# Kernel tuning notes

Measured on AMD Instinct MI355X. Metric: run time of the kernel, lower is better.

## Reference

```python
import jax, jax.numpy as jnp
import numpy as np

EMB = 1024
HEADS = 16
HEAD_DIM = EMB // HEADS
EPS = 1e-5


def gelu_tanh(x):
    c = jnp.sqrt(jnp.asarray(2.0 / jnp.pi, x.dtype))
    return 0.5 * x * (1.0 + jnp.tanh(c * (x + 0.044715 * x ** 3)))


def layernorm(x, scale, shift):
    mean = jnp.mean(x, axis=-1, keepdims=True)
    var = jnp.mean((x - mean) ** 2, axis=-1, keepdims=True)  # unbiased=False
    return scale * (x - mean) / jnp.sqrt(var + EPS) + shift


def setup_inputs() -> dict:
    key = jax.random.key(0)
    ks = jax.random.split(key, 12)
    d, dff = EMB, 4 * EMB
    sd = 1.0 / np.sqrt(d)
    inp = {
        "x": jax.random.normal(ks[0], (2, 2048, d), jnp.float32),
        "Wq": jax.random.normal(ks[1], (d, d), jnp.float32) * sd,
        "Wk": jax.random.normal(ks[2], (d, d), jnp.float32) * sd,
        "Wv": jax.random.normal(ks[3], (d, d), jnp.float32) * sd,
        "Wo": jax.random.normal(ks[4], (d, d), jnp.float32) * sd,
        "bo": jnp.zeros((d,), jnp.float32),
        "W1": jax.random.normal(ks[5], (d, dff), jnp.float32) * sd,
        "b1": jnp.zeros((dff,), jnp.float32),
        "W2": jax.random.normal(ks[6], (dff, d), jnp.float32) * (1.0 / np.sqrt(dff)),
        "b2": jnp.zeros((d,), jnp.float32),
        "g1": jnp.ones((d,), jnp.float32),
        "s1": jnp.zeros((d,), jnp.float32),
        "g2": jnp.ones((d,), jnp.float32),
        "s2": jnp.zeros((d,), jnp.float32),
    }
    return inp


def attention(x, Wq, Wk, Wv, Wo, bo):
    b, s, d = x.shape
    def heads(W):
        return (x @ W).reshape(b, s, HEADS, HEAD_DIM).transpose(0, 2, 1, 3)  # b h s hd
    q, k, v = heads(Wq), heads(Wk), heads(Wv)
    scores = jnp.einsum("bhqd,bhkd->bhqk", q, k)
    causal = jnp.tril(jnp.ones((s, s), bool))
    scores = jnp.where(causal, scores, -jnp.inf)
    w = jax.nn.softmax(scores / np.sqrt(HEAD_DIM), axis=-1)
    ctx = jnp.einsum("bhqk,bhkd->bqhd", w, v).reshape(b, s, d)
    return ctx @ Wo + bo


def reference(x, Wq, Wk, Wv, Wo, bo, W1, b1, W2, b2, g1, s1, g2, s2):
    h = x + attention(layernorm(x, g1, s1), Wq, Wk, Wv, Wo, bo)
    y = layernorm(h, g2, s2)
    y = gelu_tanh(y @ W1 + b1) @ W2 + b2
    return h + y
```

## Files before the change

kernel.cpp:

```cpp
#include <hip/hip_runtime.h>
#include <hip/hip_bf16.h>
#include <stdint.h>
#include <math.h>

#define EMB   1024
#define QS    3072
#define DFF   4096
#define HEADS 16
#define HD    64
#define BATCH 2
#define SEQ   2048
#define ROWS  (BATCH * SEQ)

typedef __hip_bfloat16 bf16;
typedef short bf16x8_t __attribute__((ext_vector_type(8)));
typedef float f32x4_t __attribute__((ext_vector_type(4)));

typedef const uint32_t __attribute__((address_space(1)))* gp_t;
typedef uint32_t __attribute__((address_space(3)))* lp_t;

__device__ __forceinline__ void async_copy16(const bf16* g, short* l) {
    __builtin_amdgcn_global_load_lds((gp_t)(const void*)g, (lp_t)(void*)l, 16, 0, 0);
}

__device__ __forceinline__ void wait_lds() {
    __asm__ volatile("" ::: "memory");
    __builtin_amdgcn_s_waitcnt(0xC07F);
    __asm__ volatile("" ::: "memory");
}

__device__ __forceinline__ float gelu_f(float x) {
    float z = 0.7978845608028654f * (x + 0.044715f * x * x * x);
    float e = __builtin_amdgcn_exp2f(z * 2.885390081777927f);
    float t = 1.0f - 2.0f * __builtin_amdgcn_rcpf(e + 1.0f);
    return 0.5f * x * (1.0f + t);
}

__device__ __forceinline__ short bf16_bits(float x) {
    bf16 b = (bf16)x;
    short s;
    __builtin_memcpy(&s, &b, 2);
    return s;
}

__device__ __forceinline__ bf16x8_t load8(const bf16* p) {
    bf16x8_t v;
    __builtin_memcpy(&v, p, 16);
    return v;
}

template<int EPI, int BM, int BK>
__global__ __launch_bounds__(256) void gemm_k(
    const bf16* __restrict__ A, const bf16* __restrict__ BT,
    bf16* __restrict__ outB, float* __restrict__ outF,
    const float* __restrict__ bias, const float* __restrict__ resF,
    int N, int K, int gxs, int cxn)
{
    __shared__ alignas(16) short As[2][BM * BK];
    __shared__ alignas(16) short Bs[2][128 * BK];
    constexpr int AI  = BM / 32;
    constexpr int KS  = BK / 32;
    constexpr int CPR = BK / 8;
    constexpr int AIS = (BM * BK) / 2048;
    constexpr int BIS = (128 * BK) / 2048;
    const int tid  = threadIdx.x;
    const int wave = tid >> 6;
    const int lane = tid & 63;
    const int quad = lane >> 4;
    const int l16  = lane & 15;

    const int q8  = (int)gridDim.x >> 3;
    const int xcd = (int)blockIdx.x & 7;
    const int l2  = (int)blockIdx.x >> 3;
    const int cx  = xcd % cxn, cy = xcd / cxn;
    const int bx  = cx * gxs + l2 % gxs;
    const int by  = cy * (q8 / gxs) + l2 / gxs;
    const int m0 = by * BM;
    const int n0 = bx * 128;
    const int wm = (wave >> 1) * (BM / 2);
    const int wn = (wave & 1) * 64;

    const bf16* Ag[AIS]; int aoff[AIS];
    const bf16* Bg[BIS]; int boff[BIS];
    #pragma unroll
    for (int i = 0; i < AIS; i++) {
        const int c = i * 256 + tid;
        const int row = c / CPR, pc = c % CPR;
        const int lch = (BK == 64) ? (pc ^ (row & 7)) : (pc ^ ((row >> 1) & 3));
        Ag[i]   = A + (size_t)(m0 + row) * K + lch * 8;
        aoff[i] = (i * 256 + wave * 64) * 8;
    }
    #pragma unroll
    for (int i = 0; i < BIS; i++) {
        const int c = i * 256 + tid;
        const int row = c / CPR, pc = c % CPR;
        const int lch = (BK == 64) ? (pc ^ (row & 7)) : (pc ^ ((row >> 1) & 3));
        Bg[i]   = BT + (size_t)(n0 + row) * K + lch * 8;
        boff[i] = (i * 256 + wave * 64) * 8;
    }

    f32x4_t acc[AI][4] = {};

    #pragma unroll
    for (int i = 0; i < AIS; i++) async_copy16(Ag[i], &As[0][aoff[i]]);
    #pragma unroll
    for (int i = 0; i < BIS; i++) async_copy16(Bg[i], &Bs[0][boff[i]]);
    __syncthreads();

    int cur = 0;
    for (int k0 = 0; k0 < K; k0 += BK) {
        const int kn = k0 + BK;
        if (kn < K) {
            #pragma unroll
            for (int i = 0; i < AIS; i++) async_copy16(Ag[i] + kn, &As[cur ^ 1][aoff[i]]);
            #pragma unroll
            for (int i = 0; i < BIS; i++) async_copy16(Bg[i] + kn, &Bs[cur ^ 1][boff[i]]);
        }
        bf16x8_t a[AI][KS], b[4][KS];
        #pragma unroll
        for (int ks = 0; ks < KS; ks++) {
            #pragma unroll
            for (int i = 0; i < AI; i++) {
                const int r = wm + i * 16 + l16;
                const int s = ks * 4 + quad;
                const int ph = (BK == 64) ? (s ^ (r & 7)) : (s ^ ((r >> 1) & 3));
                a[i][ks] = *(const bf16x8_t*)&As[cur][r * BK + ph * 8];
            }
            #pragma unroll
            for (int j = 0; j < 4; j++) {
                const int r = wn + j * 16 + l16;
                const int s = ks * 4 + quad;
                const int ph = (BK == 64) ? (s ^ (r & 7)) : (s ^ ((r >> 1) & 3));
                b[j][ks] = *(const bf16x8_t*)&Bs[cur][r * BK + ph * 8];
            }
        }
        #pragma unroll
        for (int ks = 0; ks < KS; ks++)
            #pragma unroll
            for (int i = 0; i < AI; i++)
                #pragma unroll
                for (int j = 0; j < 4; j++)
                    acc[i][j] = __builtin_amdgcn_mfma_f32_16x16x32_bf16(
                        a[i][ks], b[j][ks], acc[i][j], 0, 0, 0);
        __syncthreads();
        cur ^= 1;
    }

    #pragma unroll
    for (int j = 0; j < 4; j++) {
        const int col = n0 + wn + j * 16 + l16;
        float bv = 0.0f;
        if constexpr (EPI != 0) bv = bias[col];
        #pragma unroll
        for (int i = 0; i < AI; i++) {
            #pragma unroll
            for (int r = 0; r < 4; r++) {
                const int row = m0 + wm + i * 16 + quad * 4 + r;
                float v = acc[i][j][r] + bv;
                if constexpr (EPI == 1 || EPI == 3) {
                    v += resF[(size_t)row * N + col];
                    outF[(size_t)row * N + col] = v;
                } else if constexpr (EPI == 2) {
                    outB[(size_t)row * N + col] = (bf16)gelu_f(v);
                } else {
                    outB[(size_t)row * N + col] = (bf16)v;
                }
            }
        }
    }
}

__global__ __launch_bounds__(256) void ln_k(
    const float* __restrict__ x, const float* __restrict__ g,
    const float* __restrict__ s, bf16* __restrict__ out)
{
    const int row = blockIdx.x;
    const int t = threadIdx.x;
    const size_t base = (size_t)row * EMB + t * 4;
    float v[4];
    #pragma unroll
    for (int e = 0; e < 4; e++) v[e] = x[base + e];
    float sum = v[0] + v[1] + v[2] + v[3];
    float sq  = v[0]*v[0] + v[1]*v[1] + v[2]*v[2] + v[3]*v[3];
    #pragma unroll
    for (int o = 1; o < 64; o <<= 1) {
        sum += __shfl_xor(sum, o);
        sq  += __shfl_xor(sq, o);
    }
    __shared__ float ssum[4], ssq[4];
    const int wave = t >> 6;
    if ((t & 63) == 0) { ssum[wave] = sum; ssq[wave] = sq; }
    __syncthreads();
    sum = ssum[0] + ssum[1] + ssum[2] + ssum[3];
    sq  = ssq[0] + ssq[1] + ssq[2] + ssq[3];
    const float mean = sum * (1.0f / EMB);
    const float var  = sq * (1.0f / EMB) - mean * mean;
    const float rstd = rsqrtf(var + 1e-5f);
    #pragma unroll
    for (int e = 0; e < 4; e++)
        out[base + e] = (bf16)(g[t * 4 + e] * (v[e] - mean) * rstd + s[t * 4 + e]);
}

__global__ __launch_bounds__(256) void transpose_k(
    const float* __restrict__ src, bf16* __restrict__ dst, int R, int C)
{
    __shared__ bf16 tile[64][65];
    const int tx = threadIdx.x, ty = threadIdx.y;
    const int r0 = blockIdx.y * 64, c0 = blockIdx.x * 64;
    #pragma unroll
    for (int i = 0; i < 16; i++) {
        int r = ty + i * 4;
        tile[r][tx] = (bf16)src[(size_t)(r0 + r) * C + c0 + tx];
    }
    __syncthreads();
    #pragma unroll
    for (int i = 0; i < 16; i++) {
        int c = ty + i * 4;
        dst[(size_t)(c0 + c) * R + r0 + tx] = tile[tx][c];
    }
}

__global__ __launch_bounds__(256) void transpose3_k(
    const float* __restrict__ s0, const float* __restrict__ s1,
    const float* __restrict__ s2, bf16* __restrict__ dst, int R, int C)
{
    __shared__ bf16 tile[64][65];
    const float* src = blockIdx.z == 0 ? s0 : (blockIdx.z == 1 ? s1 : s2);
    bf16* d = dst + (size_t)blockIdx.z * R * C;
    const int tx = threadIdx.x, ty = threadIdx.y;
    const int r0 = blockIdx.y * 64, c0 = blockIdx.x * 64;
    #pragma unroll
    for (int i = 0; i < 16; i++) {
        int r = ty + i * 4;
        tile[r][tx] = (bf16)src[(size_t)(r0 + r) * C + c0 + tx];
    }
    __syncthreads();
    #pragma unroll
    for (int i = 0; i < 16; i++) {
        int c = ty + i * 4;
        d[(size_t)(c0 + c) * R + r0 + tx] = tile[tx][c];
    }
}

__global__ __launch_bounds__(256) void transpose_v_k(
    const bf16* __restrict__ src, bf16* __restrict__ dst)
{
    __shared__ bf16 tile[64][65];
    const int tx = threadIdx.x, ty = threadIdx.y;
    const int r0 = blockIdx.y * 64, c0 = blockIdx.x * 64;
    const size_t so = (size_t)blockIdx.z * SEQ * QS;
    const size_t do_ = (size_t)blockIdx.z * EMB * SEQ;
    #pragma unroll
    for (int i = 0; i < 16; i++) {
        int r = ty + i * 4;
        tile[r][tx] = src[so + (size_t)(r0 + r) * QS + c0 + tx];
    }
    __syncthreads();
    #pragma unroll
    for (int i = 0; i < 16; i++) {
        int c = ty + i * 4;
        dst[do_ + (size_t)(c0 + c) * SEQ + r0 + tx] = tile[tx][c];
    }
}

__global__ __launch_bounds__(256) void attn_k(
    const bf16* __restrict__ qkv, const bf16* __restrict__ vt,
    bf16* __restrict__ ctx)
{
    __shared__ alignas(16) short Ks[2][64 * 64];
    __shared__ alignas(16) short Vs[2][64 * 64];
    __shared__ alignas(16) short P[4][16 * 40];
    const int tid = threadIdx.x;
    const int wv = tid >> 6;
    const int lane = tid & 63;
    const int quad = lane >> 4, l16 = lane & 15;

    const int fid = (int)blockIdx.x;
    const int lid = (fid & 7) * 64 + (fid >> 3);
    const int p = lid & 15;
    const int h = (lid >> 4) & 15;
    const int b = lid >> 8;
    const size_t rowBase = (size_t)b * SEQ;

    const bf16* kcol  = qkv + 1024 + rowBase * QS + h * HD;
    const bf16* vbase = vt + (size_t)(b * HEADS + h) * HD * SEQ;

    int krw[2], kgc[2];
    #pragma unroll
    for (int i = 0; i < 2; i++) {
        const int c = i * 256 + tid;
        krw[i] = c >> 3;
        kgc[i] = (c & 7) ^ (krw[i] & 7);
    }
    const int ldsOff[2] = { (0 * 256 + wv * 64) * 8, (1 * 256 + wv * 64) * 8 };

    constexpr float SC = 0.125f * 1.44269504088896f;

    #pragma unroll
    for (int i = 0; i < 2; i++) {
        async_copy16(kcol + (size_t)krw[i] * QS + kgc[i] * 8, &Ks[0][ldsOff[i]]);
        async_copy16(vbase + (size_t)krw[i] * SEQ + kgc[i] * 8, &Vs[0][ldsOff[i]]);
    }
    __syncthreads();

    int cur = 0;
    #pragma unroll
    for (int g = 0; g < 2; g++) {
        const int chunk = g ? p : (31 - p);
        const int NK = chunk + 1;
        const int qb = chunk * 64 + wv * 16;

        bf16x8_t aq[2];
        #pragma unroll
        for (int s2 = 0; s2 < 2; s2++)
            aq[s2] = load8(&qkv[(rowBase + qb + l16) * QS + h * HD + s2 * 32 + quad * 8]);

        f32x4_t O[4] = {};
        float l_p[4] = {};

        for (int kb = 0; kb < NK; ++kb) {
            const int kbase = kb * 64;
            const bool more = (kb + 1 < NK) || (g == 0);
            if (more) {
                const int nb = (kb + 1 < NK) ? kbase + 64 : 0;
                #pragma unroll
                for (int i = 0; i < 2; i++) {
                    async_copy16(kcol + (size_t)(nb + krw[i]) * QS + kgc[i] * 8,
                                 &Ks[cur ^ 1][ldsOff[i]]);
                    async_copy16(vbase + (size_t)krw[i] * SEQ + nb + kgc[i] * 8,
                                 &Vs[cur ^ 1][ldsOff[i]]);
                }
            }
            bf16x8_t ck[4][2];
            #pragma unroll
            for (int nt = 0; nt < 4; nt++) {
                const int kr = nt * 16 + l16;
                #pragma unroll
                for (int s2 = 0; s2 < 2; s2++)
                    ck[nt][s2] = *(const bf16x8_t*)
                        &Ks[cur][kr * 64 + (((s2 * 4 + quad) ^ (kr & 7)) << 3)];
            }
            f32x4_t sc[4] = {};
            __builtin_amdgcn_s_setprio(1);
            #pragma unroll
            for (int nt = 0; nt < 4; nt++)
                #pragma unroll
                for (int s2 = 0; s2 < 2; s2++)
                    sc[nt] = __builtin_amdgcn_mfma_f32_16x16x32_bf16(
                        aq[s2], ck[nt][s2], sc[nt], 0, 0, 0);
            __builtin_amdgcn_s_setprio(0);

            short* Pw = P[wv];
            const bool full = (kbase + 63 <= qb);
            #pragma unroll
            for (int hf = 0; hf < 2; hf++) {
                bf16x8_t cv[4];
                #pragma unroll
                for (int c = 0; c < 4; c++) {
                    const int vr = c * 16 + l16;
                    cv[c] = *(const bf16x8_t*)
                        &Vs[cur][vr * 64 + (((hf * 4 + quad) ^ (vr & 7)) << 3)];
                }
                if (full) {
                    #pragma unroll
                    for (int nt2 = 0; nt2 < 2; nt2++) {
                        const int nt = hf * 2 + nt2;
                        #pragma unroll
                        for (int r = 0; r < 4; r++) {
                            const float pe = __builtin_amdgcn_exp2f(sc[nt][r] * SC);
                            l_p[r] += pe;
                            Pw[(quad * 4 + r) * 40 + nt2 * 16 + l16] = bf16_bits(pe);
                        }
                    }
                } else {
                    #pragma unroll
                    for (int nt2 = 0; nt2 < 2; nt2++) {
                        const int nt = hf * 2 + nt2;
                        const int kk = kbase + nt * 16 + l16;
                        #pragma unroll
                        for (int r = 0; r < 4; r++) {
                            const int qg = qb + quad * 4 + r;
                            float s = sc[nt][r] * SC;
                            if (kk > qg) s = -1e30f;
                            const float pe = __builtin_amdgcn_exp2f(s);
                            l_p[r] += pe;
                            Pw[(quad * 4 + r) * 40 + nt2 * 16 + l16] = bf16_bits(pe);
                        }
                    }
                }
                wait_lds();
                bf16x8_t pa = *(const bf16x8_t*)&Pw[l16 * 40 + quad * 8];
                __builtin_amdgcn_s_setprio(1);
                #pragma unroll
                for (int c = 0; c < 4; c++)
                    O[c] = __builtin_amdgcn_mfma_f32_16x16x32_bf16(pa, cv[c], O[c], 0, 0, 0);
                __builtin_amdgcn_s_setprio(0);
            }
            __syncthreads();
            cur ^= 1;
        }

        #pragma unroll
        for (int r = 0; r < 4; r++) {
            float l = l_p[r];
            l += __shfl_xor(l, 1);
            l += __shfl_xor(l, 2);
            l += __shfl_xor(l, 4);
            l += __shfl_xor(l, 8);
            const float inv = 1.0f / l;
            #pragma unroll
            for (int c = 0; c < 4; c++)
                ctx[(rowBase + qb + quad * 4 + r) * EMB + h * HD + c * 16 + l16]
                    = (bf16)(O[c][r] * inv);
        }
    }
}

extern "C" void kernel_launch(void* const* d_in, const int* in_sizes, int n_in,
                              void* d_out, int out_size, void* d_ws, size_t ws_size,
                              hipStream_t stream) {
    const float* X  = (const float*)d_in[0];
    const float* Wq = (const float*)d_in[1];
    const float* Wk = (const float*)d_in[2];
    const float* Wv = (const float*)d_in[3];
    const float* Wo = (const float*)d_in[4];
    const float* bo = (const float*)d_in[5];
    const float* W1 = (const float*)d_in[6];
    const float* b1 = (const float*)d_in[7];
    const float* W2 = (const float*)d_in[8];
    const float* b2 = (const float*)d_in[9];
    const float* g1 = (const float*)d_in[10];
    const float* s1 = (const float*)d_in[11];
    const float* g2 = (const float*)d_in[12];
    const float* s2 = (const float*)d_in[13];
    float* out = (float*)d_out;

    char* ws = (char*)d_ws;
    const size_t MB = 1024 * 1024;
    bf16*  lnbuf = (bf16*)(ws + 0);
    bf16*  qkv   = (bf16*)(ws + 8 * MB);
    bf16*  vtb   = (bf16*)(ws + 32 * MB);
    bf16*  ctx   = (bf16*)(ws + 40 * MB);
    float* hbuf  = (float*)(ws + 48 * MB);
    bf16*  WqT   = (bf16*)(ws + 64 * MB);
    bf16*  WoT   = (bf16*)(ws + 70 * MB);
    bf16*  ffn1  = (bf16*)(ws + 8 * MB);
    bf16*  W1T   = (bf16*)(ws + 40 * MB);
    bf16*  W2T   = (bf16*)(ws + 64 * MB);

    const dim3 tb(64, 4);
    transpose3_k<<<dim3(16, 16, 3), tb, 0, stream>>>(Wq, Wk, Wv, WqT, EMB, EMB);
    transpose_k<<<dim3(16, 16, 1), tb, 0, stream>>>(Wo, WoT, EMB, EMB);

    ln_k<<<ROWS, 256, 0, stream>>>(X, g1, s1, lnbuf);

    gemm_k<0, 128, 32><<<768, 256, 0, stream>>>(
        lnbuf, WqT, qkv, nullptr, nullptr, nullptr, QS, EMB, 12, 2);

    transpose_v_k<<<dim3(16, 32, BATCH), tb, 0, stream>>>(qkv + 2048, vtb);

    attn_k<<<512, 256, 0, stream>>>(qkv, vtb, ctx);

    gemm_k<1, 64, 64><<<512, 256, 0, stream>>>(
        ctx, WoT, nullptr, hbuf, bo, X, EMB, EMB, 8, 1);

    transpose_k<<<dim3(64, 16, 1), tb, 0, stream>>>(W1, W1T, EMB, DFF);
    transpose_k<<<dim3(16, 64, 1), tb, 0, stream>>>(W2, W2T, DFF, EMB);

    ln_k<<<ROWS, 256, 0, stream>>>(hbuf, g2, s2, lnbuf);

    gemm_k<2, 128, 32><<<1024, 256, 0, stream>>>(
        lnbuf, W1T, ffn1, nullptr, b1, nullptr, DFF, EMB, 16, 2);

    gemm_k<3, 64, 64><<<512, 256, 0, stream>>>(
        ffn1, W2T, nullptr, out, b2, hbuf, EMB, DFF, 8, 1);
}
```

Baseline: 346.7 us.

## Add triple-buffered LDS pipeline with vmcnt waits for BM=128 GEMMs

Adds a DEEP template path to the GEMM kernel that uses three LDS buffers and prefetches two K-tiles ahead. Each iteration waits only on the older async loads using s_waitcnt vmcnt, followed by a raw barrier, so there is one barrier per iteration. The goal is to hide global-load latency in the QKV and FFN1 GEMMs. The cost is 50% more LDS per block, which may reduce occupancy, and a dependence on hand-encoded waitcnt values being correct.

Result: no change. 348.1 us (+0.4%).

```diff
diff --git a/kernel.cpp b/kernel.cpp
--- a/kernel.cpp
+++ b/kernel.cpp
@@ -49,20 +49,22 @@
     return v;
 }
 
-template<int EPI, int BM, int BK>
+template<int EPI, int BM, int BK, bool DEEP>
 __global__ __launch_bounds__(256) void gemm_k(
     const bf16* __restrict__ A, const bf16* __restrict__ BT,
     bf16* __restrict__ outB, float* __restrict__ outF,
     const float* __restrict__ bias, const float* __restrict__ resF,
     int N, int K, int gxs, int cxn)
 {
-    __shared__ alignas(16) short As[2][BM * BK];
-    __shared__ alignas(16) short Bs[2][128 * BK];
+    constexpr int NBUF = DEEP ? 3 : 2;
+    __shared__ alignas(16) short As[NBUF][BM * BK];
+    __shared__ alignas(16) short Bs[NBUF][128 * BK];
     constexpr int AI  = BM / 32;
     constexpr int KS  = BK / 32;
     constexpr int CPR = BK / 8;
     constexpr int AIS = (BM * BK) / 2048;
     constexpr int BIS = (128 * BK) / 2048;
+    constexpr int NV  = AIS + BIS;
     const int tid  = threadIdx.x;
     const int wave = tid >> 6;
     const int lane = tid & 63;
@@ -101,49 +103,113 @@
 
     f32x4_t acc[AI][4] = {};
 
-    #pragma unroll
-    for (int i = 0; i < AIS; i++) async_copy16(Ag[i], &As[0][aoff[i]]);
-    #pragma unroll
-    for (int i = 0; i < BIS; i++) async_copy16(Bg[i], &Bs[0][boff[i]]);
-    __syncthreads();
-
-    int cur = 0;
-    for (int k0 = 0; k0 < K; k0 += BK) {
-        const int kn = k0 + BK;
-        if (kn < K) {
-            #pragma unroll
-            for (int i = 0; i < AIS; i++) async_copy16(Ag[i] + kn, &As[cur ^ 1][aoff[i]]);
-            #pragma unroll
-            for (int i = 0; i < BIS; i++) async_copy16(Bg[i] + kn, &Bs[cur ^ 1][boff[i]]);
+    if constexpr (DEEP) {
+        const int T = K / BK;
+        #pragma unroll
+        for (int i = 0; i < AIS; i++) async_copy16(Ag[i], &As[0][aoff[i]]);
+        #pragma unroll
+        for (int i = 0; i < BIS; i++) async_copy16(Bg[i], &Bs[0][boff[i]]);
+        #pragma unroll
+        for (int i = 0; i < AIS; i++) async_copy16(Ag[i] + BK, &As[1][aoff[i]]);
+        #pragma unroll
+        for (int i = 0; i < BIS; i++) async_copy16(Bg[i] + BK, &Bs[1][boff[i]]);
+
+        __asm__ volatile("" ::: "memory");
+        __builtin_amdgcn_s_waitcnt(0x0F70 | NV);
+        __builtin_amdgcn_s_barrier();
+        __asm__ volatile("" ::: "memory");
+
+        int cb = 0;
+        for (int t = 0; t < T; ++t) {
+            if (t + 2 < T) {
+                const int sb = (cb == 0) ? 2 : cb - 1;
+                const int k0 = (t + 2) * BK;
+                #pragma unroll
+                for (int i = 0; i < AIS; i++) async_copy16(Ag[i] + k0, &As[sb][aoff[i]]);
+                #pragma unroll
+                for (int i = 0; i < BIS; i++) async_copy16(Bg[i] + k0, &Bs[sb][boff[i]]);
+            }
+            bf16x8_t a[AI][KS], b[4][KS];
+            #pragma unroll
+            for (int ks = 0; ks < KS; ks++) {
+                #pragma unroll
+                for (int i = 0; i < AI; i++) {
+                    const int r = wm + i * 16 + l16;
+                    const int s = ks * 4 + quad;
+                    const int ph = (BK == 64) ? (s ^ (r & 7)) : (s ^ ((r >> 1) & 3));
+                    a[i][ks] = *(const bf16x8_t*)&As[cb][r * BK + ph * 8];
+                }
+                #pragma unroll
+                for (int j = 0; j < 4; j++) {
+                    const int r = wn + j * 16 + l16;
+                    const int s = ks * 4 + quad;
+                    const int ph = (BK == 64) ? (s ^ (r & 7)) : (s ^ ((r >> 1) & 3));
+                    b[j][ks] = *(const bf16x8_t*)&Bs[cb][r * BK + ph * 8];
+                }
+            }
+            #pragma unroll
+            for (int ks = 0; ks < KS; ks++)
+                #pragma unroll
+                for (int i = 0; i < AI; i++)
+                    #pragma unroll
+                    for (int j = 0; j < 4; j++)
+                        acc[i][j] = __builtin_amdgcn_mfma_f32_16x16x32_bf16(
+                            a[i][ks], b[j][ks], acc[i][j], 0, 0, 0);
+
+            if (t + 1 < T) {
+                __asm__ volatile("" ::: "memory");
+                if (t + 2 < T) __builtin_amdgcn_s_waitcnt(0x0F70 | NV);
+                else           __builtin_amdgcn_s_waitcnt(0x0F70);
+                __builtin_amdgcn_s_barrier();
+                __asm__ volatile("" ::: "memory");
+            }
+            cb = (cb == 2) ? 0 : cb + 1;
         }
-        bf16x8_t a[AI][KS], b[4][KS];
-        #pragma unroll
-        for (int ks = 0; ks < KS; ks++) {
-            #pragma unroll
-            for (int i = 0; i < AI; i++) {
-                const int r = wm + i * 16 + l16;
-                const int s = ks * 4 + quad;
-                const int ph = (BK == 64) ? (s ^ (r & 7)) : (s ^ ((r >> 1) & 3));
-                a[i][ks] = *(const bf16x8_t*)&As[cur][r * BK + ph * 8];
-            }
-            #pragma unroll
-            for (int j = 0; j < 4; j++) {
-                const int r = wn + j * 16 + l16;
-                const int s = ks * 4 + quad;
-                const int ph = (BK == 64) ? (s ^ (r & 7)) : (s ^ ((r >> 1) & 3));
-                b[j][ks] = *(const bf16x8_t*)&Bs[cur][r * BK + ph * 8];
-            }
+    } else {
+        #pragma unroll
+        for (int i = 0; i < AIS; i++) async_copy16(Ag[i], &As[0][aoff[i]]);
+        #pragma unroll
+        for (int i = 0; i < BIS; i++) async_copy16(Bg[i], &Bs[0][boff[i]]);
+        __syncthreads();
+
+        int cur = 0;
+        for (int k0 = 0; k0 < K; k0 += BK) {
+            const int kn = k0 + BK;
+            if (kn < K) {
+                #pragma unroll
+                for (int i = 0; i < AIS; i++) async_copy16(Ag[i] + kn, &As[cur ^ 1][aoff[i]]);
+                #pragma unroll
+                for (int i = 0; i < BIS; i++) async_copy16(Bg[i] + kn, &Bs[cur ^ 1][boff[i]]);
+            }
+            bf16x8_t a[AI][KS], b[4][KS];
+            #pragma unroll
+            for (int ks = 0; ks < KS; ks++) {
+                #pragma unroll
+                for (int i = 0; i < AI; i++) {
+                    const int r = wm + i * 16 + l16;
+                    const int s = ks * 4 + quad;
+                    const int ph = (BK == 64) ? (s ^ (r & 7)) : (s ^ ((r >> 1) & 3));
+                    a[i][ks] = *(const bf16x8_t*)&As[cur][r * BK + ph * 8];
+                }
+                #pragma unroll
+                for (int j = 0; j < 4; j++) {
+                    const int r = wn + j * 16 + l16;
+                    const int s = ks * 4 + quad;
+                    const int ph = (BK == 64) ? (s ^ (r & 7)) : (s ^ ((r >> 1) & 3));
+                    b[j][ks] = *(const bf16x8_t*)&Bs[cur][r * BK + ph * 8];
+                }
+            }
+            #pragma unroll
+            for (int ks = 0; ks < KS; ks++)
+                #pragma unroll
+                for (int i = 0; i < AI; i++)
+                    #pragma unroll
+                    for (int j = 0; j < 4; j++)
+                        acc[i][j] = __builtin_amdgcn_mfma_f32_16x16x32_bf16(
+                            a[i][ks], b[j][ks], acc[i][j], 0, 0, 0);
+            __syncthreads();
+            cur ^= 1;
         }
-        #pragma unroll
-        for (int ks = 0; ks < KS; ks++)
-            #pragma unroll
-            for (int i = 0; i < AI; i++)
-                #pragma unroll
-                for (int j = 0; j < 4; j++)
-                    acc[i][j] = __builtin_amdgcn_mfma_f32_16x16x32_bf16(
-                        a[i][ks], b[j][ks], acc[i][j], 0, 0, 0);
-        __syncthreads();
-        cur ^= 1;
     }
 
     #pragma unroll
@@ -454,14 +520,14 @@
 
     ln_k<<<ROWS, 256, 0, stream>>>(X, g1, s1, lnbuf);
 
-    gemm_k<0, 128, 32><<<768, 256, 0, stream>>>(
+    gemm_k<0, 128, 32, true><<<768, 256, 0, stream>>>(
         lnbuf, WqT, qkv, nullptr, nullptr, nullptr, QS, EMB, 12, 2);
 
     transpose_v_k<<<dim3(16, 32, BATCH), tb, 0, stream>>>(qkv + 2048, vtb);
 
     attn_k<<<512, 256, 0, stream>>>(qkv, vtb, ctx);
 
-    gemm_k<1, 64, 64><<<512, 256, 0, stream>>>(
+    gemm_k<1, 64, 64, false><<<512, 256, 0, stream>>>(
         ctx, WoT, nullptr, hbuf, bo, X, EMB, EMB, 8, 1);
 
     transpose_k<<<dim3(64, 16, 1), tb, 0, stream>>>(W1, W1T, EMB, DFF);
@@ -469,9 +535,9 @@
 
     ln_k<<<ROWS, 256, 0, stream>>>(hbuf, g2, s2, lnbuf);
 
-    gemm_k<2, 128, 32><<<1024, 256, 0, stream>>>(
+    gemm_k<2, 128, 32, true><<<1024, 256, 0, stream>>>(
         lnbuf, W1T, ffn1, nullptr, b1, nullptr, DFF, EMB, 16, 2);
 
-    gemm_k<3, 64, 64><<<512, 256, 0, stream>>>(
+    gemm_k<3, 64, 64, false><<<512, 256, 0, stream>>>(
         ffn1, W2T, nullptr, out, b2, hbuf, EMB, DFF, 8, 1);
 }
```
